# Kernel tuning notes

Measured on AMD Instinct MI355X. Metric: run time of the kernel, lower is better.

Reference implementation:

```python
import jax, jax.numpy as jnp
import numpy as np


def setup_inputs() -> dict:
    key = jax.random.key(0)
    x = jax.random.normal(key, (4, 3, 8192), dtype=jnp.float32)  # (B, 3, N)
    return {"x": x, "k": 30}


def reference(x, k):
    # x: (B, 3, N)
    x_t = jnp.swapaxes(x, 1, 2)  # (B, N, 3)
    xx = jnp.sum(x_t ** 2, axis=2, keepdims=True)  # (B, N, 1)
    # pairwise squared distances (B, N, N)
    pairwise = xx + jnp.swapaxes(xx, 1, 2) - 2.0 * jnp.matmul(x_t, x)
    # k smallest distances -> negate and take top_k
    _, idx = jax.lax.top_k(-pairwise, k)  # idx: (B, N, k)
    # gather neighbors: (B, N, k, 3)
    neighbors = jax.vmap(lambda pts, i: pts[i])(x_t, idx)
    centroid = jnp.mean(neighbors, axis=2, keepdims=True)  # (B, N, 1, 3)
    centered = neighbors - centroid  # (B, N, k, 3)
    # per-point 3x3 covariance
    cov = jnp.einsum('bnki,bnkj->bnij', centered, centered)  # (B, N, 3, 3)
    _, v = jnp.linalg.eigh(cov)  # eigenvalues ascending
    normals = v[..., :, 0]  # eigenvector of smallest eigenvalue, (B, N, 3)
    # orient normals toward viewpoint (origin): view_dir = -x_t
    dot = jnp.sum(-x_t * normals, axis=-1, keepdims=True)
    normals = jnp.where(dot < 0, -normals, normals)
    x_out = jnp.concatenate([x, jnp.swapaxes(normals, 1, 2)], axis=1)  # (B, 6, N)
    return x_out
```

## Files before the change

### kernel.cpp

```cpp
#include <hip/hip_runtime.h>
#include <math.h>

#define N_PTS   8192
#define KNN     30
#define CAPG    104
#define STR     105
#define GROUPS  8
#define BLOCK   128
#define NZ      64
#define NY      64
#define NBKT    (NZ * NY)
#define CLO     -4.0f
#define CSC     8.0f
#define LAMBDA  48.0f


__device__ __forceinline__ int clampi(int v, int lo, int hi) {
    return v < lo ? lo : (v > hi ? hi : v);
}
__device__ __forceinline__ int bucket_of(float pz, float py) {
    int zb = clampi((int)floorf((pz - CLO) * CSC), 0, NZ - 1);
    int yb = clampi((int)floorf((py - CLO) * CSC), 0, NY - 1);
    return (zb << 6) | yb;
}

__global__ __launch_bounds__(1024) void prep_kernel(const float* __restrict__ x,
                                                    float4* __restrict__ S,
                                                    int* __restrict__ O,
                                                    int* __restrict__ bstart,
                                                    float* __restrict__ out) {
    __shared__ int hist[NBKT];
    __shared__ int cur[NBKT];
    __shared__ int wsum[16];

    const int b = blockIdx.x;
    const int t = threadIdx.x;
    const int wid = t >> 6, lane = t & 63;
    const float* xb = x + (size_t)b * 3 * N_PTS;
    float* ob = out + (size_t)b * 6 * N_PTS;

    for (int k = t; k < NBKT; k += 1024) hist[k] = 0;
    __syncthreads();

    float px[8], py[8], pz[8];
    int   bk[8];
    #pragma unroll
    for (int u = 0; u < 8; ++u) {
        int i = (u << 10) + t;
        px[u] = xb[i]; py[u] = xb[N_PTS + i]; pz[u] = xb[2 * N_PTS + i];
        bk[u] = bucket_of(pz[u], py[u]);
        atomicAdd(&hist[bk[u]], 1);
        ob[i]             = px[u];
        ob[N_PTS + i]     = py[u];
        ob[2 * N_PTS + i] = pz[u];
    }
    __syncthreads();

    int l0 = hist[4 * t], l1 = hist[4 * t + 1], l2 = hist[4 * t + 2], l3 = hist[4 * t + 3];
    int s = l0 + l1 + l2 + l3;
    int sum = s;
    #pragma unroll
    for (int off = 1; off < 64; off <<= 1) {
        int v = __shfl_up(sum, off);
        if (lane >= off) sum += v;
    }
    if (lane == 63) wsum[wid] = sum;
    __syncthreads();
    if (t == 0) {
        int run = 0;
        #pragma unroll
        for (int k = 0; k < 16; ++k) { int v = wsum[k]; wsum[k] = run; run += v; }
    }
    __syncthreads();
    int base = wsum[wid] + (sum - s);
    int b0 = base, b1 = base + l0, b2 = b1 + l1, b3 = b2 + l2;
    cur[4 * t] = b0; cur[4 * t + 1] = b1; cur[4 * t + 2] = b2; cur[4 * t + 3] = b3;
    int* bsb = bstart + b * (NBKT + 1);
    bsb[4 * t] = b0; bsb[4 * t + 1] = b1; bsb[4 * t + 2] = b2; bsb[4 * t + 3] = b3;
    if (t == 1023) bsb[NBKT] = N_PTS;
    __syncthreads();

    float4* Sb = S + ((size_t)b << 13);
    int*    Ob = O + ((size_t)b << 13);
    #pragma unroll
    for (int u = 0; u < 8; ++u) {
        int dst = atomicAdd(&cur[bk[u]], 1);
        float xx = __fadd_rn(__fadd_rn(__fmul_rn(px[u], px[u]), __fmul_rn(py[u], py[u])),
                             __fmul_rn(pz[u], pz[u]));
        Sb[dst] = make_float4(px[u], py[u], pz[u], xx);
        Ob[dst] = (u << 10) + t;
    }
}

__global__ __launch_bounds__(BLOCK, 6) void knn_normal_kernel(const float4* __restrict__ S,
                                                              const int* __restrict__ O,
                                                              const int* __restrict__ bstart,
                                                              float* __restrict__ out) {
    __shared__ unsigned long long ldk[GROUPS * STR];

    const int t    = threadIdx.x;
    const int l16  = t & 15;
    const int g    = t >> 4;
    const int gsh  = (t & 63) & ~15;
    const int qblk = (blockIdx.x * 1031) & 4095;
    const int qid  = qblk * GROUPS + g;
    const int b    = qid >> 13;
    const int pos  = qid & (N_PTS - 1);
    const float4* __restrict__ P  = S + ((size_t)b << 13);
    const int*    __restrict__ Ob = O + ((size_t)b << 13);
    const int*    __restrict__ bs = bstart + b * (NBKT + 1);
    const float4 qp = P[pos];
    const int    oi = Ob[pos];

    unsigned long long* __restrict__ ldg = ldk + g * STR;

    const float c = fmaxf(sqrtf(qp.w), 1e-3f);
    float rlo = 0.05f, rhi = 6.0f;
    for (int it = 0; it < 14; ++it) {
        float r = 0.5f * (rlo + rhi);
        float slo = fmaxf(c - r, 0.0f);
        float h = (c + r - slo) * 0.125f;
        float f = 0.0f;
        if (l16 <= 8) {
            float sq = slo + h * (float)l16;
            float cs = c - sq;
            float hh = fmaxf(fminf((r * r - cs * cs) * (0.5f / c), 2.0f * sq), 0.0f);
            float w = (l16 == 0 || l16 == 8) ? 1.0f : ((l16 & 1) ? 4.0f : 2.0f);
            f = w * __expf(-0.5f * sq * sq) * sq * hh;
        }
        f += __shfl_xor(f, 1, 16); f += __shfl_xor(f, 2, 16);
        f += __shfl_xor(f, 4, 16); f += __shfl_xor(f, 8, 16);
        float lam = 1089.3f * f * h;
        if (lam < LAMBDA) rlo = r; else rhi = r;
    }
    float rad = rhi * 1.02f;
    float r2  = rad * rad;

    int  cnt = 0;
    bool active = true;

    for (;;) {
        if (active) {
            cnt = 0;
            float w = __fmaf_rn(sqrtf(r2), 1.002f, 1e-3f);
            int zlo = clampi((int)floorf((qp.z - w - CLO) * CSC), 0, NZ - 1);
            int zhi = clampi((int)floorf((qp.z + w - CLO) * CSC), 0, NZ - 1);
            int ylo = clampi((int)floorf((qp.y - w - CLO) * CSC), 0, NY - 1);
            int yhi = clampi((int)floorf((qp.y + w - CLO) * CSC), 0, NY - 1);
            for (int zb = zlo; zb <= zhi; ++zb) {
                int lo = bs[(zb << 6) + ylo];
                int hi = bs[(zb << 6) + yhi + 1];
                int smax = (hi - lo + 31) >> 5;
                for (int s = 0; s < smax; ++s) {
                    int j1  = lo + (s << 5) + l16;
                    int j2  = j1 + 16;
                    int jc1 = j1 < hi ? j1 : hi - 1;
                    int jc2 = j2 < hi ? j2 : hi - 1;
                    float4 p1 = P[jc1];
                    float4 p2 = P[jc2];
                    float mm1 = __fmaf_rn(qp.z, p1.z, __fmaf_rn(qp.y, p1.y, __fmul_rn(qp.x, p1.x)));
                    float d1  = __fsub_rn(__fadd_rn(qp.w, p1.w), __fmul_rn(2.0f, mm1));
                    float mm2 = __fmaf_rn(qp.z, p2.z, __fmaf_rn(qp.y, p2.y, __fmul_rn(qp.x, p2.x)));
                    float d2  = __fsub_rn(__fadd_rn(qp.w, p2.w), __fmul_rn(2.0f, mm2));
                    bool hit1 = (j1 < hi) && (d1 <= r2);
                    bool hit2 = (j2 < hi) && (d2 <= r2);
                    unsigned long long m1 = __ballot(hit1);
                    unsigned sub1 = (unsigned)((m1 >> gsh) & 0xFFFFull);
                    if (hit1) {
                        int slot = cnt + __popc(sub1 & ((1u << l16) - 1u));
                        if (slot < CAPG) {
                            unsigned u = __float_as_uint(d1);
                            u = (u & 0x80000000u) ? ~u : (u | 0x80000000u);
                            ldg[slot] = ((unsigned long long)u << 28) | (unsigned long long)jc1;
                        }
                    }
                    cnt += __popc(sub1);
                    unsigned long long m2 = __ballot(hit2);
                    unsigned sub2 = (unsigned)((m2 >> gsh) & 0xFFFFull);
                    if (hit2) {
                        int slot = cnt + __popc(sub2 & ((1u << l16) - 1u));
                        if (slot < CAPG) {
                            unsigned u = __float_as_uint(d2);
                            u = (u & 0x80000000u) ? ~u : (u | 0x80000000u);
                            ldg[slot] = ((unsigned long long)u << 28) | (unsigned long long)jc2;
                        }
                    }
                    cnt += __popc(sub2);
                }
            }
        }
        bool bad = active && (cnt < KNN || cnt > CAPG);
        if (__ballot(bad) == 0ULL) break;
        active = bad;
        if (active) r2 = (cnt < KNN) ? r2 * 1.6f : r2 * 0.82f;
    }

    for (int k = l16; k < cnt; k += 16) {
        unsigned long long key = ldg[k];
        int jc = (int)(key & 0x3FFFull);
        ldg[k] = (key & ~0x0FFFFFFFull) | ((unsigned long long)Ob[jc] << 14) | (unsigned long long)jc;
    }
    __syncthreads();

    const double qx = (double)qp.x, qy = (double)qp.y, qz = (double)qp.z;
    double sx = 0.0, sy = 0.0, sz = 0.0;
    double sxx = 0.0, sxy = 0.0, sxz = 0.0, syy = 0.0, syz = 0.0, szz = 0.0;

    for (int k = l16; k < cnt; k += 16) {
        unsigned long long key = ldg[k];
        int rank = 0;
        for (int u = 0; u < cnt; ++u) rank += (ldg[u] < key) ? 1 : 0;
        if (rank < KNN) {
            float4 p = P[(int)(key & 0x3FFFull)];
            double ax = (double)p.x - qx, ay = (double)p.y - qy, az = (double)p.z - qz;
            sx += ax; sy += ay; sz += az;
            sxx = fma(ax, ax, sxx); sxy = fma(ax, ay, sxy); sxz = fma(ax, az, sxz);
            syy = fma(ay, ay, syy); syz = fma(ay, az, syz); szz = fma(az, az, szz);
        }
    }

    #pragma unroll
    for (int off = 1; off < 16; off <<= 1) {
        sx  += __shfl_xor(sx,  off, 16); sy  += __shfl_xor(sy,  off, 16); sz  += __shfl_xor(sz,  off, 16);
        sxx += __shfl_xor(sxx, off, 16); sxy += __shfl_xor(sxy, off, 16); sxz += __shfl_xor(sxz, off, 16);
        syy += __shfl_xor(syy, off, 16); syz += __shfl_xor(syz, off, 16); szz += __shfl_xor(szz, off, 16);
    }

    if (l16 == 0) {
        const double kinv = 1.0 / (double)KNN;
        double m00 = sxx - sx * sx * kinv;
        double m11 = syy - sy * sy * kinv;
        double m22 = szz - sz * sz * kinv;
        double m01 = sxy - sx * sy * kinv;
        double m02 = sxz - sx * sz * kinv;
        double m12 = syz - sy * sz * kinv;

        double nx = 1.0, ny = 0.0, nz = 0.0;
        double q3 = (m00 + m11 + m22) / 3.0;
        double p1 = m01 * m01 + m02 * m02 + m12 * m12;
        double d00 = m00 - q3, d11 = m11 - q3, d22 = m22 - q3;
        double p2 = d00 * d00 + d11 * d11 + d22 * d22 + 2.0 * p1;
        if (p2 > 1e-280) {
            double pp = sqrt(p2 / 6.0);
            double ip = 1.0 / pp;
            double b00 = d00 * ip, b11 = d11 * ip, b22 = d22 * ip;
            double b01 = m01 * ip, b02 = m02 * ip, b12 = m12 * ip;
            double detB = b00 * (b11 * b22 - b12 * b12)
                        - b01 * (b01 * b22 - b12 * b02)
                        + b02 * (b01 * b12 - b11 * b02);
            double rr = 0.5 * detB;
            rr = rr < -1.0 ? -1.0 : (rr > 1.0 ? 1.0 : rr);
            double phi = acos(rr) / 3.0;
            double lam = q3 + 2.0 * pp * cos(phi + 2.0943951023931953);
            double a00 = m00 - lam, a11 = m11 - lam, a22 = m22 - lam;
            double v0x = m01 * m12 - m02 * a11, v0y = m02 * m01 - a00 * m12, v0z = a00 * a11 - m01 * m01;
            double v1x = m01 * a22 - m02 * m12, v1y = m02 * m02 - a00 * a22, v1z = a00 * m12 - m01 * m02;
            double v2x = a11 * a22 - m12 * m12, v2y = m12 * m02 - m01 * a22, v2z = m01 * m12 - a11 * m02;
            double n0 = v0x * v0x + v0y * v0y + v0z * v0z;
            double n1 = v1x * v1x + v1y * v1y + v1z * v1z;
            double n2 = v2x * v2x + v2y * v2y + v2z * v2z;
            double bx = v0x, by = v0y, bz = v0z, bn = n0;
            if (n1 > bn) { bx = v1x; by = v1y; bz = v1z; bn = n1; }
            if (n2 > bn) { bx = v2x; by = v2y; bz = v2z; bn = n2; }
            if (bn > 1e-280) {
                double inv = 1.0 / sqrt(bn);
                nx = bx * inv; ny = by * inv; nz = bz * inv;
            }
        }
        double dq = -(qx * nx + qy * ny + qz * nz);
        if (dq < 0.0) { nx = -nx; ny = -ny; nz = -nz; }

        float* ob = out + (size_t)b * 6 * N_PTS;
        ob[3 * N_PTS + oi] = (float)nx;
        ob[4 * N_PTS + oi] = (float)ny;
        ob[5 * N_PTS + oi] = (float)nz;
    }
}

extern "C" void kernel_launch(void* const* d_in, const int* in_sizes, int n_in,
                              void* d_out, int out_size, void* d_ws, size_t ws_size,
                              hipStream_t stream) {
    const float* x = (const float*)d_in[0];
    float* out = (float*)d_out;
    char* ws = (char*)d_ws;
    float4* S    = (float4*)(ws);
    int*    O    = (int*)(ws + 524288);
    int*    bsta = (int*)(ws + 655360);

    prep_kernel<<<dim3(4), dim3(1024), 0, stream>>>(x, S, O, bsta, out);
    knn_normal_kernel<<<dim3(32768 / GROUPS), dim3(BLOCK), 0, stream>>>(S, O, bsta, out);
}
```

Measured before the change: 164.4 us.

## Split prep into parallel hist/scan/scatter kernels and register-resident rank selection

The single 4-block prep kernel is split into a 128-block histogram kernel using global atomics, a per-batch scan kernel and a 128-block scatter kernel, with a memset clearing the global histogram first. This spreads the prep work across many more CUs at the cost of extra launches and global atomics. The kNN kernel now holds up to 7 candidate keys per lane in registers and computes their ranks in one pass over LDS, with a cheaper path when the candidate count is at most 64, and it replaces a block-wide barrier with a wave barrier. The radius bisection also drops from 14 to 12 iterations, which makes the radius estimate less precise and may trigger more of the retry loop.

```diff
diff --git a/kernel.cpp b/kernel.cpp
--- a/kernel.cpp
+++ b/kernel.cpp
@@ -14,6 +14,11 @@
 #define CSC     8.0f
 #define LAMBDA  48.0f
 
+#define WS_S   0
+#define WS_O   524288
+#define WS_BS  655360
+#define WS_GH  720912
+#define WS_GC  786448
 
 __device__ __forceinline__ int clampi(int v, int lo, int hi) {
     return v < lo ? lo : (v > hi ? hi : v);
@@ -24,39 +29,31 @@
     return (zb << 6) | yb;
 }
 
-__global__ __launch_bounds__(1024) void prep_kernel(const float* __restrict__ x,
-                                                    float4* __restrict__ S,
-                                                    int* __restrict__ O,
-                                                    int* __restrict__ bstart,
-                                                    float* __restrict__ out) {
-    __shared__ int hist[NBKT];
-    __shared__ int cur[NBKT];
+__global__ __launch_bounds__(256) void prep_hist_kernel(const float* __restrict__ x,
+                                                        float* __restrict__ out,
+                                                        int* __restrict__ ghist) {
+    const int i = blockIdx.x * 256 + threadIdx.x;
+    const int b = i >> 13;
+    const int p = i & (N_PTS - 1);
+    const float* xb = x + (size_t)b * 3 * N_PTS;
+    float* ob = out + (size_t)b * 6 * N_PTS;
+    float px = xb[p], py = xb[N_PTS + p], pz = xb[2 * N_PTS + p];
+    ob[p]             = px;
+    ob[N_PTS + p]     = py;
+    ob[2 * N_PTS + p] = pz;
+    atomicAdd(&ghist[(b << 12) + bucket_of(pz, py)], 1);
+}
+
+__global__ __launch_bounds__(1024) void prep_scan_kernel(const int* __restrict__ ghist,
+                                                         int* __restrict__ bstart,
+                                                         int* __restrict__ gcur) {
     __shared__ int wsum[16];
-
     const int b = blockIdx.x;
     const int t = threadIdx.x;
     const int wid = t >> 6, lane = t & 63;
-    const float* xb = x + (size_t)b * 3 * N_PTS;
-    float* ob = out + (size_t)b * 6 * N_PTS;
-
-    for (int k = t; k < NBKT; k += 1024) hist[k] = 0;
-    __syncthreads();
-
-    float px[8], py[8], pz[8];
-    int   bk[8];
-    #pragma unroll
-    for (int u = 0; u < 8; ++u) {
-        int i = (u << 10) + t;
-        px[u] = xb[i]; py[u] = xb[N_PTS + i]; pz[u] = xb[2 * N_PTS + i];
-        bk[u] = bucket_of(pz[u], py[u]);
-        atomicAdd(&hist[bk[u]], 1);
-        ob[i]             = px[u];
-        ob[N_PTS + i]     = py[u];
-        ob[2 * N_PTS + i] = pz[u];
-    }
-    __syncthreads();
-
-    int l0 = hist[4 * t], l1 = hist[4 * t + 1], l2 = hist[4 * t + 2], l3 = hist[4 * t + 3];
+    const int* gh = ghist + (b << 12);
+
+    int l0 = gh[4 * t], l1 = gh[4 * t + 1], l2 = gh[4 * t + 2], l3 = gh[4 * t + 3];
     int s = l0 + l1 + l2 + l3;
     int sum = s;
     #pragma unroll
@@ -74,22 +71,28 @@
     __syncthreads();
     int base = wsum[wid] + (sum - s);
     int b0 = base, b1 = base + l0, b2 = b1 + l1, b3 = b2 + l2;
-    cur[4 * t] = b0; cur[4 * t + 1] = b1; cur[4 * t + 2] = b2; cur[4 * t + 3] = b3;
     int* bsb = bstart + b * (NBKT + 1);
+    int* gc  = gcur + (b << 12);
     bsb[4 * t] = b0; bsb[4 * t + 1] = b1; bsb[4 * t + 2] = b2; bsb[4 * t + 3] = b3;
+    gc[4 * t]  = b0; gc[4 * t + 1]  = b1; gc[4 * t + 2]  = b2; gc[4 * t + 3]  = b3;
     if (t == 1023) bsb[NBKT] = N_PTS;
-    __syncthreads();
-
-    float4* Sb = S + ((size_t)b << 13);
-    int*    Ob = O + ((size_t)b << 13);
-    #pragma unroll
-    for (int u = 0; u < 8; ++u) {
-        int dst = atomicAdd(&cur[bk[u]], 1);
-        float xx = __fadd_rn(__fadd_rn(__fmul_rn(px[u], px[u]), __fmul_rn(py[u], py[u])),
-                             __fmul_rn(pz[u], pz[u]));
-        Sb[dst] = make_float4(px[u], py[u], pz[u], xx);
-        Ob[dst] = (u << 10) + t;
-    }
+}
+
+__global__ __launch_bounds__(256) void prep_scatter_kernel(const float* __restrict__ x,
+                                                           float4* __restrict__ S,
+                                                           int* __restrict__ O,
+                                                           int* __restrict__ gcur) {
+    const int i = blockIdx.x * 256 + threadIdx.x;
+    const int b = i >> 13;
+    const int p = i & (N_PTS - 1);
+    const float* xb = x + (size_t)b * 3 * N_PTS;
+    float px = xb[p], py = xb[N_PTS + p], pz = xb[2 * N_PTS + p];
+    int bk = bucket_of(pz, py);
+    int dst = atomicAdd(&gcur[(b << 12) + bk], 1);
+    float xx = __fadd_rn(__fadd_rn(__fmul_rn(px, px), __fmul_rn(py, py)),
+                         __fmul_rn(pz, pz));
+    S[((size_t)b << 13) + dst] = make_float4(px, py, pz, xx);
+    O[((size_t)b << 13) + dst] = p;
 }
 
 __global__ __launch_bounds__(BLOCK, 6) void knn_normal_kernel(const float4* __restrict__ S,
@@ -116,7 +119,7 @@
 
     const float c = fmaxf(sqrtf(qp.w), 1e-3f);
     float rlo = 0.05f, rhi = 6.0f;
-    for (int it = 0; it < 14; ++it) {
+    for (int it = 0; it < 12; ++it) {
         float r = 0.5f * (rlo + rhi);
         float slo = fmaxf(c - r, 0.0f);
         float h = (c + r - slo) * 0.125f;
@@ -195,29 +198,47 @@
         if (active) r2 = (cnt < KNN) ? r2 * 1.6f : r2 * 0.82f;
     }
 
-    for (int k = l16; k < cnt; k += 16) {
-        unsigned long long key = ldg[k];
-        int jc = (int)(key & 0x3FFFull);
-        ldg[k] = (key & ~0x0FFFFFFFull) | ((unsigned long long)Ob[jc] << 14) | (unsigned long long)jc;
-    }
-    __syncthreads();
+    unsigned long long k0 = ~0ULL, k1 = ~0ULL, k2 = ~0ULL, k3 = ~0ULL,
+                       k4 = ~0ULL, k5 = ~0ULL, k6 = ~0ULL;
+    #define FILLK(J, KV) { int idx = l16 + 16 * (J); if (idx < cnt) {            \
+        unsigned long long key = ldg[idx];                                       \
+        int jc = (int)(key & 0x3FFFull);                                         \
+        KV = (key & ~0x0FFFFFFFull) | ((unsigned long long)Ob[jc] << 14)         \
+             | (unsigned long long)jc;                                           \
+        ldg[idx] = KV; } }
+    FILLK(0, k0) FILLK(1, k1) FILLK(2, k2) FILLK(3, k3)
+    FILLK(4, k4) FILLK(5, k5) FILLK(6, k6)
+    #undef FILLK
+    __builtin_amdgcn_wave_barrier();
+
+    int r0 = 0, r1 = 0, r2i = 0, r3 = 0, r4 = 0, r5 = 0, r6 = 0;
+    if (cnt <= 64) {
+        for (int u = 0; u < cnt; ++u) {
+            unsigned long long ku = ldg[u];
+            r0 += ku < k0; r1 += ku < k1; r2i += ku < k2; r3 += ku < k3;
+        }
+        r4 = r5 = r6 = KNN;
+    } else {
+        for (int u = 0; u < cnt; ++u) {
+            unsigned long long ku = ldg[u];
+            r0 += ku < k0; r1 += ku < k1; r2i += ku < k2; r3 += ku < k3;
+            r4 += ku < k4; r5 += ku < k5; r6 += ku < k6;
+        }
+    }
 
     const double qx = (double)qp.x, qy = (double)qp.y, qz = (double)qp.z;
     double sx = 0.0, sy = 0.0, sz = 0.0;
     double sxx = 0.0, sxy = 0.0, sxz = 0.0, syy = 0.0, syz = 0.0, szz = 0.0;
 
-    for (int k = l16; k < cnt; k += 16) {
-        unsigned long long key = ldg[k];
-        int rank = 0;
-        for (int u = 0; u < cnt; ++u) rank += (ldg[u] < key) ? 1 : 0;
-        if (rank < KNN) {
-            float4 p = P[(int)(key & 0x3FFFull)];
-            double ax = (double)p.x - qx, ay = (double)p.y - qy, az = (double)p.z - qz;
-            sx += ax; sy += ay; sz += az;
-            sxx = fma(ax, ax, sxx); sxy = fma(ax, ay, sxy); sxz = fma(ax, az, sxz);
-            syy = fma(ay, ay, syy); syz = fma(ay, az, syz); szz = fma(az, az, szz);
-        }
-    }
+    #define ACCJ(KV, RV) if ((RV) < KNN) {                                       \
+        float4 p = P[(int)((KV) & 0x3FFFull)];                                   \
+        double ax = (double)p.x - qx, ay = (double)p.y - qy, az = (double)p.z - qz; \
+        sx += ax; sy += ay; sz += az;                                            \
+        sxx = fma(ax, ax, sxx); sxy = fma(ax, ay, sxy); sxz = fma(ax, az, sxz);  \
+        syy = fma(ay, ay, syy); syz = fma(ay, az, syz); szz = fma(az, az, szz); }
+    ACCJ(k0, r0) ACCJ(k1, r1) ACCJ(k2, r2i) ACCJ(k3, r3)
+    ACCJ(k4, r4) ACCJ(k5, r5) ACCJ(k6, r6)
+    #undef ACCJ
 
     #pragma unroll
     for (int off = 1; off < 16; off <<= 1) {
@@ -283,10 +304,15 @@
     const float* x = (const float*)d_in[0];
     float* out = (float*)d_out;
     char* ws = (char*)d_ws;
-    float4* S    = (float4*)(ws);
-    int*    O    = (int*)(ws + 524288);
-    int*    bsta = (int*)(ws + 655360);
-
-    prep_kernel<<<dim3(4), dim3(1024), 0, stream>>>(x, S, O, bsta, out);
-    knn_normal_kernel<<<dim3(32768 / GROUPS), dim3(BLOCK), 0, stream>>>(S, O, bsta, out);
-}
+    float4* S    = (float4*)(ws + WS_S);
+    int*    O    = (int*)(ws + WS_O);
+    int*    bsta = (int*)(ws + WS_BS);
+    int*    gh   = (int*)(ws + WS_GH);
+    int*    gc   = (int*)(ws + WS_GC);
+
+    hipMemsetAsync(gh, 0, 4 * NBKT * sizeof(int), stream);
+    prep_hist_kernel   <<<dim3(128), dim3(256),  0, stream>>>(x, out, gh);
+    prep_scan_kernel   <<<dim3(4),   dim3(1024), 0, stream>>>(gh, bsta, gc);
+    prep_scatter_kernel<<<dim3(128), dim3(256),  0, stream>>>(x, S, O, gc);
+    knn_normal_kernel  <<<dim3(32768 / GROUPS), dim3(BLOCK), 0, stream>>>(S, O, bsta, out);
+}
```

Result: slower. 170.9 us (+3.9%).
